# Optimization experiments

Hardware: AMD Instinct MI355X
Metric: run time of the kernel (lower is better)

## Reference

```python
import jax, jax.numpy as jnp
import numpy as np

ALPHA = 0.1
K = 10


def setup_inputs() -> dict:
    key = jax.random.key(0)
    ks = jax.random.split(key, 8)
    N, E, F_IN, H, C = 100000, 1600000, 256, 128, 16
    features = jax.random.normal(ks[0], (N, F_IN), dtype=jnp.float32)
    # Kaiming-ish small init so activations stay sane
    W0 = jax.random.normal(ks[1], (F_IN, H), dtype=jnp.float32) * (1.0 / np.sqrt(F_IN))
    b0 = jnp.zeros((H,), jnp.float32)
    W1 = jax.random.normal(ks[2], (H, H), dtype=jnp.float32) * (1.0 / np.sqrt(H))
    b1 = jnp.zeros((H,), jnp.float32)
    W2 = jax.random.normal(ks[3], (H, C), dtype=jnp.float32) * (1.0 / np.sqrt(H))
    b2 = jnp.zeros((C,), jnp.float32)
    src = jax.random.randint(ks[4], (E,), 0, N, dtype=jnp.int32)
    dst = jax.random.randint(ks[5], (E,), 0, N, dtype=jnp.int32)
    return {"features": features, "W0": W0, "b0": b0, "W1": W1, "b1": b1,
            "W2": W2, "b2": b2, "src": src, "dst": dst}


def reference(features, W0, b0, W1, b1, W2, b2, src, dst):
    N = features.shape[0]
    # --- MLP feature transform (feat_drop=0 -> identity) ---
    h = jax.nn.relu(features @ W0 + b0)
    h = jax.nn.relu(h @ W1 + b1)
    h = h @ W2 + b2  # [N, C]
    # --- symmetric normalization D_out^{-1/2} A D_in^{-1/2} (DGL APPNPConv) ---
    ones = jnp.ones(src.shape[0], dtype=h.dtype)
    out_deg = jax.ops.segment_sum(ones, src, num_segments=N)
    in_deg = jax.ops.segment_sum(ones, dst, num_segments=N)
    norm_src = jnp.where(out_deg > 0, jax.lax.rsqrt(jnp.maximum(out_deg, 1.0)), 0.0)[:, None]
    norm_dst = jnp.where(in_deg > 0, jax.lax.rsqrt(jnp.maximum(in_deg, 1.0)), 0.0)[:, None]
    # --- K-step personalized PageRank propagation (edge_drop=0) ---
    h0 = h
    for _ in range(K):
        msg = (h * norm_src)[src]                         # gather [E, C]
        agg = jax.ops.segment_sum(msg, dst, num_segments=N)  # scatter-add [N, C]
        h = (1.0 - ALPHA) * (agg * norm_dst) + ALPHA * h0
    return h
```

## Files before the change

### kernel.cpp

```cpp
#include <hip/hip_runtime.h>

typedef _Float16 half8 __attribute__((ext_vector_type(8)));
typedef _Float16 half4 __attribute__((ext_vector_type(4)));
typedef float f32x4 __attribute__((ext_vector_type(4)));
typedef unsigned short u16;
typedef unsigned char u8;
typedef unsigned int u32;

constexpr int F_IN = 256;
constexpr int H    = 128;
constexpr int C    = 16;
constexpr int KITER = 10;

constexpr int RANGE = 32768;
constexpr int PCH   = 128;


__global__ __launch_bounds__(256) void hist_k(const int* __restrict__ idx,
                                              u8* __restrict__ partial,
                                              int N, int E, int R, int chunk) {
    __shared__ unsigned int cnt[RANGE / 4];
    const int p  = blockIdx.x / R;
    const int r  = blockIdx.x % R;
    const int lo = r * RANGE;
    const int hi = min(lo + RANGE, N);
    const int t  = threadIdx.x;
    for (int i = t; i < RANGE / 4; i += 256) cnt[i] = 0;
    __syncthreads();
    const int e0 = p * chunk, e1 = min(e0 + chunk, E);
    for (int e = e0 + t; e < e1; e += 256) {
        int d = idx[e];
        if (d >= lo && d < hi) {
            int dl = d - lo;
            atomicAdd(&cnt[dl >> 2], 1u << ((dl & 3) << 3));
        }
    }
    __syncthreads();
    const int nw = (hi - lo) >> 2;
    u8* prow = partial + (size_t)p * N + lo;
    for (int k = t; k < nw; k += 256)
        *reinterpret_cast<u32*>(prow + k * 4) = cnt[k];
    for (int i = lo + nw * 4 + t; i < hi; i += 256) {
        int il = i - lo;
        partial[(size_t)p * N + i] = (u8)(cnt[il >> 2] >> ((il & 3) << 3));
    }
}

__global__ __launch_bounds__(256) void hist_rank_k(const int* __restrict__ idx,
                                                   u8* __restrict__ partial,
                                                   u8* __restrict__ rank8,
                                                   int N, int E, int R, int chunk) {
    __shared__ unsigned int cnt[RANGE / 4];
    const int p  = blockIdx.x / R;
    const int r  = blockIdx.x % R;
    const int lo = r * RANGE;
    const int hi = min(lo + RANGE, N);
    const int t  = threadIdx.x;
    for (int i = t; i < RANGE / 4; i += 256) cnt[i] = 0;
    __syncthreads();
    const int e0 = p * chunk, e1 = min(e0 + chunk, E);
    for (int e = e0 + t; e < e1; e += 256) {
        int d = idx[e];
        if (d >= lo && d < hi) {
            int dl    = d - lo;
            int shift = (dl & 3) << 3;
            unsigned int old = atomicAdd(&cnt[dl >> 2], 1u << shift);
            rank8[e] = (u8)((old >> shift) & 0xffu);
        }
    }
    __syncthreads();
    const int nw = (hi - lo) >> 2;
    u8* prow = partial + (size_t)p * N + lo;
    for (int k = t; k < nw; k += 256)
        *reinterpret_cast<u32*>(prow + k * 4) = cnt[k];
    for (int i = lo + nw * 4 + t; i < hi; i += 256) {
        int il = i - lo;
        partial[(size_t)p * N + i] = (u8)(cnt[il >> 2] >> ((il & 3) << 3));
    }
}


__global__ __launch_bounds__(256) void colsum4_k(const u8* __restrict__ partial,
                                                 int* __restrict__ deg, int NG, int N) {
    int q = blockIdx.x * 256 + threadIdx.x;
    if (q >= NG) return;
    int i0 = q * 4;
    if (i0 + 4 <= N) {
        int s0 = 0, s1 = 0, s2 = 0, s3 = 0;
#pragma unroll 8
        for (int p = 0; p < PCH; ++p) {
            uchar4 v = *reinterpret_cast<const uchar4*>(partial + (size_t)p * N + i0);
            s0 += v.x; s1 += v.y; s2 += v.z; s3 += v.w;
        }
        *reinterpret_cast<int4*>(deg + i0) = make_int4(s0, s1, s2, s3);
    } else {
        for (int i = i0; i < N; ++i) {
            int s = 0;
            for (int p = 0; p < PCH; ++p) s += partial[(size_t)p * N + i];
            deg[i] = s;
        }
    }
}


__global__ __launch_bounds__(256) void colprefix_norm_scan4_k(u8* __restrict__ partial,
                                                              const int* __restrict__ dego,
                                                              float* __restrict__ ns,
                                                              float* __restrict__ nd,
                                                              int* __restrict__ off,
                                                              int* __restrict__ bsum,
                                                              int NG, int N) {
    __shared__ int s[256];
    int t = threadIdx.x, q = blockIdx.x * 256 + t;
    int r0 = 0, r1 = 0, r2 = 0, r3 = 0;
    int i0 = q * 4;
    bool full = (q < NG) && (i0 + 4 <= N);
    if (full) {
        for (int p = 0; p < PCH; ++p) {
            size_t base = (size_t)p * N + i0;
            uchar4 v = *reinterpret_cast<const uchar4*>(partial + base);
            uchar4 w; w.x = (u8)r0; w.y = (u8)r1; w.z = (u8)r2; w.w = (u8)r3;
            *reinterpret_cast<uchar4*>(partial + base) = w;
            r0 += v.x; r1 += v.y; r2 += v.z; r3 += v.w;
        }
        int4 dg = *reinterpret_cast<const int4*>(dego + i0);
        float4 nsv, ndv;
        nsv.x = (dg.x > 0) ? rsqrtf((float)dg.x) : 0.0f;
        nsv.y = (dg.y > 0) ? rsqrtf((float)dg.y) : 0.0f;
        nsv.z = (dg.z > 0) ? rsqrtf((float)dg.z) : 0.0f;
        nsv.w = (dg.w > 0) ? rsqrtf((float)dg.w) : 0.0f;
        ndv.x = (r0 > 0) ? rsqrtf((float)r0) : 0.0f;
        ndv.y = (r1 > 0) ? rsqrtf((float)r1) : 0.0f;
        ndv.z = (r2 > 0) ? rsqrtf((float)r2) : 0.0f;
        ndv.w = (r3 > 0) ? rsqrtf((float)r3) : 0.0f;
        *reinterpret_cast<float4*>(ns + i0) = nsv;
        *reinterpret_cast<float4*>(nd + i0) = ndv;
    } else if (q < NG) {
        int rr[4] = {0, 0, 0, 0};
        int nn = N - i0;
        for (int p = 0; p < PCH; ++p) {
            for (int j = 0; j < nn; ++j) {
                size_t qq = (size_t)p * N + i0 + j;
                int v = partial[qq];
                partial[qq] = (u8)rr[j];
                rr[j] += v;
            }
        }
        for (int j = 0; j < nn; ++j) {
            int a = dego[i0 + j];
            ns[i0 + j] = (a > 0) ? rsqrtf((float)a) : 0.0f;
            nd[i0 + j] = (rr[j] > 0) ? rsqrtf((float)rr[j]) : 0.0f;
        }
        r0 = rr[0]; r1 = rr[1]; r2 = rr[2]; r3 = rr[3];
    }
    int tot = r0 + r1 + r2 + r3;
    s[t] = (q < NG) ? tot : 0;
    __syncthreads();
    for (int dd = 1; dd < 256; dd <<= 1) {
        int x = (t >= dd) ? s[t - dd] : 0;
        __syncthreads();
        s[t] += x;
        __syncthreads();
    }
    if (q < NG) {
        int ex = s[t] - tot;
        if (i0 + 4 <= N) {
            int4 o;
            o.x = ex; o.y = ex + r0; o.z = ex + r0 + r1; o.w = ex + r0 + r1 + r2;
            *reinterpret_cast<int4*>(off + i0) = o;
        } else {
            int rr[4] = {r0, r1, r2, r3};
            int run = ex;
            for (int j = 0; j < N - i0; ++j) { off[i0 + j] = run; run += rr[j]; }
        }
    }
    if (t == 255) bsum[blockIdx.x] = s[255];
}

__global__ __launch_bounds__(512) void scan2(int* __restrict__ bsum, int nb) {
    __shared__ int s[512];
    int t = threadIdx.x;
    int v = (t < nb) ? bsum[t] : 0;
    s[t] = v;
    __syncthreads();
    for (int dd = 1; dd < 512; dd <<= 1) {
        int x = (t >= dd) ? s[t - dd] : 0;
        __syncthreads();
        s[t] += x;
        __syncthreads();
    }
    if (t < nb) bsum[t] = s[t] - v;
}

__global__ __launch_bounds__(256) void scan3_4(int* __restrict__ off, const int* __restrict__ bsum,
                                               int NG, int N) {
    int q = blockIdx.x * 256 + threadIdx.x;
    if (q >= NG) return;
    int b = bsum[blockIdx.x];
    int i0 = q * 4;
    if (i0 + 4 <= N) {
        int4 o = *reinterpret_cast<const int4*>(off + i0);
        o.x += b; o.y += b; o.z += b; o.w += b;
        *reinterpret_cast<int4*>(off + i0) = o;
    } else {
        for (int j = 0; j < N - i0; ++j) off[i0 + j] += b;
    }
}


__global__ __launch_bounds__(256) void scatter_pass(const int* __restrict__ src,
                                                    const int* __restrict__ dst,
                                                    const int* __restrict__ off,
                                                    const u8* __restrict__ pprefix,
                                                    const u8* __restrict__ rank8,
                                                    u32* __restrict__ epack,
                                                    int N, int E, int chunk) {
    int e = blockIdx.x * 256 + threadIdx.x;
    if (e < E) {
        int d = dst[e];
        int p = e / chunk;
        int pos = off[d] + (int)pprefix[(size_t)p * N + d] + (int)rank8[e];
        epack[pos] = (u32)src[e];
    }
}


__device__ inline void pack_one(const float* __restrict__ W, half8* __restrict__ out,
                                int tid, int NT, int Ncols) {
    int l  = tid & 63;
    int q  = tid >> 6;
    int nt = q % NT;
    int ks = q / NT;
    int col = nt * 16 + (l & 15);
    int kb  = ks * 32 + ((l >> 4) * 8);
    half8 h;
#pragma unroll
    for (int j = 0; j < 8; ++j) h[j] = (_Float16)W[(kb + j) * Ncols + col];
    out[tid] = h;
}

__global__ __launch_bounds__(256) void wpack_all(const float* __restrict__ W0,
                                                 const float* __restrict__ W1,
                                                 const float* __restrict__ W2,
                                                 half8* __restrict__ B0,
                                                 half8* __restrict__ B1,
                                                 half8* __restrict__ B2) {
    int tid = blockIdx.x * 256 + threadIdx.x;
    if (tid < 4096)      pack_one(W0, B0, tid, 8, 128);
    else if (tid < 6144) pack_one(W1, B1, tid - 4096, 8, 128);
    else if (tid < 6400) pack_one(W2, B2, tid - 6144, 1, 16);
}


__global__ __launch_bounds__(256) void mlp_direct(
    const float* __restrict__ feat,
    const half8* __restrict__ B0, const float* __restrict__ b0,
    const half8* __restrict__ B1, const float* __restrict__ b1,
    const half8* __restrict__ B2, const float* __restrict__ b2,
    const float* __restrict__ ns,
    float* __restrict__ h0out, _Float16* __restrict__ g0out, int N)
{
    __shared__ __align__(16) char lds[4 * 4096];
    const int t  = threadIdx.x;
    const int l  = t & 63;
    const int w  = t >> 6;
    const int cl = l & 15;
    const int qk = l >> 4;
    char* swp = lds + w * 4096;

    const int rowg = blockIdx.x * 64 + w * 16 + cl;
    const int rowc = (rowg < N) ? rowg : (N - 1);

    const float* ap = feat + (size_t)rowc * F_IN + qk * 8;
    float4 f[16];
#pragma unroll
    for (int i = 0; i < 16; ++i)
        f[i] = *reinterpret_cast<const float4*>(ap + (i >> 1) * 32 + (i & 1) * 4);
    __builtin_amdgcn_sched_barrier(0);

    half8 a0[8];
#pragma unroll
    for (int ks = 0; ks < 8; ++ks) {
        half8 h;
        h[0] = (_Float16)f[2 * ks].x;     h[1] = (_Float16)f[2 * ks].y;
        h[2] = (_Float16)f[2 * ks].z;     h[3] = (_Float16)f[2 * ks].w;
        h[4] = (_Float16)f[2 * ks + 1].x; h[5] = (_Float16)f[2 * ks + 1].y;
        h[6] = (_Float16)f[2 * ks + 1].z; h[7] = (_Float16)f[2 * ks + 1].w;
        a0[ks] = h;
    }

    f32x4 acc0[8];
#pragma unroll
    for (int nt = 0; nt < 8; ++nt) acc0[nt] = (f32x4){0.f, 0.f, 0.f, 0.f};
#pragma unroll
    for (int ks = 0; ks < 8; ++ks)
#pragma unroll
        for (int nt = 0; nt < 8; ++nt)
            acc0[nt] = __builtin_amdgcn_mfma_f32_16x16x32_f16(a0[ks], B0[(ks * 8 + nt) * 64 + l],
                                                              acc0[nt], 0, 0, 0);
#pragma unroll
    for (int nt = 0; nt < 8; ++nt) {
        float bb = b0[nt * 16 + cl];
#pragma unroll
        for (int r = 0; r < 4; ++r) {
            int orow = qk * 4 + r;
            int byte = orow * 256 + (((nt * 16 + cl) * 2) ^ ((orow & 7) << 4));
            *reinterpret_cast<_Float16*>(swp + byte) = (_Float16)fmaxf(acc0[nt][r] + bb, 0.0f);
        }
    }

    half8 a1[4];
#pragma unroll
    for (int ks = 0; ks < 4; ++ks) {
        int byte = cl * 256 + (((qk * 8 + ks * 32) * 2) ^ ((cl & 7) << 4));
        a1[ks] = *reinterpret_cast<const half8*>(swp + byte);
    }
    f32x4 acc1[8];
#pragma unroll
    for (int nt = 0; nt < 8; ++nt) acc1[nt] = (f32x4){0.f, 0.f, 0.f, 0.f};
#pragma unroll
    for (int ks = 0; ks < 4; ++ks)
#pragma unroll
        for (int nt = 0; nt < 8; ++nt)
            acc1[nt] = __builtin_amdgcn_mfma_f32_16x16x32_f16(a1[ks], B1[(ks * 8 + nt) * 64 + l],
                                                              acc1[nt], 0, 0, 0);
#pragma unroll
    for (int nt = 0; nt < 8; ++nt) {
        float bb = b1[nt * 16 + cl];
#pragma unroll
        for (int r = 0; r < 4; ++r) {
            int orow = qk * 4 + r;
            int byte = orow * 256 + (((nt * 16 + cl) * 2) ^ ((orow & 7) << 4));
            *reinterpret_cast<_Float16*>(swp + byte) = (_Float16)fmaxf(acc1[nt][r] + bb, 0.0f);
        }
    }

    f32x4 acc2 = (f32x4){0.f, 0.f, 0.f, 0.f};
#pragma unroll
    for (int ks = 0; ks < 4; ++ks) {
        int byte = cl * 256 + (((qk * 8 + ks * 32) * 2) ^ ((cl & 7) << 4));
        half8 a2 = *reinterpret_cast<const half8*>(swp + byte);
        acc2 = __builtin_amdgcn_mfma_f32_16x16x32_f16(a2, B2[ks * 64 + l], acc2, 0, 0, 0);
    }
    float bb2 = b2[cl];
#pragma unroll
    for (int r = 0; r < 4; ++r) {
        int orow = qk * 4 + r;
        int node = blockIdx.x * 64 + w * 16 + orow;
        if (node < N) {
            float hv = acc2[r] + bb2;
            h0out[(size_t)node * C + cl] = hv;
            g0out[(size_t)node * C + cl] = (_Float16)(hv * ns[node]);
        }
    }
}


__global__ __launch_bounds__(256) void gatherg(const u32* __restrict__ ep,
                                               const int* __restrict__ off,
                                               const half4* __restrict__ g,
                                               const float4* __restrict__ h0,
                                               const float* __restrict__ ns,
                                               const float* __restrict__ nd,
                                               half4* __restrict__ gnext,
                                               float4* __restrict__ hout,
                                               int N, int E, int last) {
    int gid = blockIdx.x * 256 + threadIdx.x;
    int node = gid >> 2;
    if (node >= N) return;
    int c = gid & 3;
    int o0 = off[node];
    int o1 = (node + 1 < N) ? off[node + 1] : E;
    float k  = 0.9f * nd[node];
    float sc = ns[node];
    float4 hv = h0[gid];
    float4 aA = {0.f, 0.f, 0.f, 0.f};
    float4 aB = {0.f, 0.f, 0.f, 0.f};
    float4 aC = {0.f, 0.f, 0.f, 0.f};
    float4 aD = {0.f, 0.f, 0.f, 0.f};
    int o = o0;
    for (; o + 8 <= o1; o += 8) {
        int s0 = (int)ep[o];     int s1 = (int)ep[o + 1];
        int s2 = (int)ep[o + 2]; int s3 = (int)ep[o + 3];
        int s4 = (int)ep[o + 4]; int s5 = (int)ep[o + 5];
        int s6 = (int)ep[o + 6]; int s7 = (int)ep[o + 7];
        half4 x0 = g[s0 * 4 + c]; half4 x1 = g[s1 * 4 + c];
        half4 x2 = g[s2 * 4 + c]; half4 x3 = g[s3 * 4 + c];
        half4 x4 = g[s4 * 4 + c]; half4 x5 = g[s5 * 4 + c];
        half4 x6 = g[s6 * 4 + c]; half4 x7 = g[s7 * 4 + c];
        aA.x += (float)x0[0]; aA.y += (float)x0[1]; aA.z += (float)x0[2]; aA.w += (float)x0[3];
        aB.x += (float)x1[0]; aB.y += (float)x1[1]; aB.z += (float)x1[2]; aB.w += (float)x1[3];
        aC.x += (float)x2[0]; aC.y += (float)x2[1]; aC.z += (float)x2[2]; aC.w += (float)x2[3];
        aD.x += (float)x3[0]; aD.y += (float)x3[1]; aD.z += (float)x3[2]; aD.w += (float)x3[3];
        aA.x += (float)x4[0]; aA.y += (float)x4[1]; aA.z += (float)x4[2]; aA.w += (float)x4[3];
        aB.x += (float)x5[0]; aB.y += (float)x5[1]; aB.z += (float)x5[2]; aB.w += (float)x5[3];
        aC.x += (float)x6[0]; aC.y += (float)x6[1]; aC.z += (float)x6[2]; aC.w += (float)x6[3];
        aD.x += (float)x7[0]; aD.y += (float)x7[1]; aD.z += (float)x7[2]; aD.w += (float)x7[3];
    }
    for (; o + 2 <= o1; o += 2) {
        int s0 = (int)ep[o];
        int s1 = (int)ep[o + 1];
        half4 x0 = g[s0 * 4 + c];
        half4 x1 = g[s1 * 4 + c];
        aA.x += (float)x0[0]; aA.y += (float)x0[1]; aA.z += (float)x0[2]; aA.w += (float)x0[3];
        aB.x += (float)x1[0]; aB.y += (float)x1[1]; aB.z += (float)x1[2]; aB.w += (float)x1[3];
    }
    if (o < o1) {
        int s0 = (int)ep[o];
        half4 x0 = g[s0 * 4 + c];
        aA.x += (float)x0[0]; aA.y += (float)x0[1]; aA.z += (float)x0[2]; aA.w += (float)x0[3];
    }
    aA.x += aB.x + aC.x + aD.x;
    aA.y += aB.y + aC.y + aD.y;
    aA.z += aB.z + aC.z + aD.z;
    aA.w += aB.w + aC.w + aD.w;
    float4 res;
    res.x = fmaf(k, aA.x, 0.1f * hv.x);
    res.y = fmaf(k, aA.y, 0.1f * hv.y);
    res.z = fmaf(k, aA.z, 0.1f * hv.z);
    res.w = fmaf(k, aA.w, 0.1f * hv.w);
    if (last) {
        hout[gid] = res;
    } else {
        half4 gv;
        gv[0] = (_Float16)(res.x * sc);
        gv[1] = (_Float16)(res.y * sc);
        gv[2] = (_Float16)(res.z * sc);
        gv[3] = (_Float16)(res.w * sc);
        gnext[gid] = gv;
    }
}


extern "C" void kernel_launch(void* const* d_in, const int* in_sizes, int n_in,
                              void* d_out, int out_size, void* d_ws, size_t ws_size,
                              hipStream_t stream) {
    const float* feat = (const float*)d_in[0];
    const float* W0   = (const float*)d_in[1];
    const float* b0   = (const float*)d_in[2];
    const float* W1   = (const float*)d_in[3];
    const float* b1   = (const float*)d_in[4];
    const float* W2   = (const float*)d_in[5];
    const float* b2   = (const float*)d_in[6];
    const int*   src  = (const int*)d_in[7];
    const int*   dst  = (const int*)d_in[8];

    const int N = in_sizes[0] / F_IN;
    const int E = in_sizes[7];
    const int R  = (N + RANGE - 1) / RANGE;
    const int chunk = (E + PCH - 1) / PCH;
    const int NG = (N + 3) / 4;
    const int NBG = (NG + 255) / 256;

    char* base = (char*)d_ws;
    u8* part = (u8*)base;
    float*    h0 = (float*)base;
    _Float16* g0 = (_Float16*)(base + (size_t)N * C * 4);
    _Float16* ga = (_Float16*)(base + (size_t)N * C * 6);
    _Float16* gb = (_Float16*)(base + (size_t)N * C * 8);
    char* ws = base + (size_t)N * C * 10;
    int*   dego = (int*)ws;   ws += (size_t)N * 4;
    float* ns   = (float*)ws; ws += (size_t)N * 4;
    float* nd   = (float*)ws; ws += (size_t)N * 4;
    int*   off  = (int*)ws;   ws += (size_t)N * 4;
    int*   bsum = (int*)ws;   ws += 512 * 4;
    u8*    rank8 = (u8*)ws;   ws += (size_t)E;
    ws = (char*)(((size_t)ws + 15) & ~(size_t)15);
    u32*   epack  = (u32*)ws; ws += (size_t)E * 4;
    half8* B0 = (half8*)ws;   ws += 4096 * 16;
    half8* B1 = (half8*)ws;   ws += 2048 * 16;
    half8* B2 = (half8*)ws;   ws += 256 * 16;

    hist_k<<<PCH * R, 256, 0, stream>>>(src, part, N, E, R, chunk);
    colsum4_k<<<NBG, 256, 0, stream>>>(part, dego, NG, N);
    hist_rank_k<<<PCH * R, 256, 0, stream>>>(dst, part, rank8, N, E, R, chunk);
    colprefix_norm_scan4_k<<<NBG, 256, 0, stream>>>(part, dego, ns, nd, off, bsum, NG, N);

    scan2<<<1, 512, 0, stream>>>(bsum, NBG);
    scan3_4<<<NBG, 256, 0, stream>>>(off, bsum, NG, N);
    scatter_pass<<<(E + 255) / 256, 256, 0, stream>>>(src, dst, off, part, rank8, epack, N, E, chunk);

    wpack_all<<<25, 256, 0, stream>>>(W0, W1, W2, B0, B1, B2);
    mlp_direct<<<(N + 63) / 64, 256, 0, stream>>>(feat, B0, b0, B1, b1, B2, b2, ns, h0, g0, N);

    const _Float16* curg = g0;
    for (int it = 0; it < KITER; ++it) {
        int last = (it == KITER - 1);
        _Float16* nxtg = (it & 1) ? gb : ga;
        gatherg<<<(N * 4 + 255) / 256, 256, 0, stream>>>(epack, off, (const half4*)curg,
                                                         (const float4*)h0, ns, nd,
                                                         (half4*)nxtg, (float4*)d_out, N, E, last);
        curg = nxtg;
    }
}
```

Baseline: 323.8 us.

## Sort nodes by in-degree to balance gather work across wavefronts

Adds a counting sort of nodes by in-degree (histogram, scan, scatter kernels) to build a permutation. The propagation gather then processes nodes in degree-sorted order, so lanes in a wavefront run similar loop trip counts and divergence is reduced. The cost is three extra setup kernels, including a serial single-block scan, plus an extra indirection and scattered writes and h0 reads in each iteration.

```diff
diff --git a/kernel.cpp b/kernel.cpp
--- a/kernel.cpp
+++ b/kernel.cpp
@@ -224,6 +224,60 @@
     }
 }
 
+__global__ __launch_bounds__(256) void dhist_k(const int* __restrict__ off,
+                                               u8* __restrict__ rankp,
+                                               int* __restrict__ pbin,
+                                               int NBLK, int N, int E) {
+    __shared__ int hist[256];
+    int t = threadIdx.x, i = blockIdx.x * 256 + t;
+    hist[t] = 0;
+    __syncthreads();
+    if (i < N) {
+        int d = ((i + 1 < N) ? off[i + 1] : E) - off[i];
+        int bin = min(d, 255);
+        int r = atomicAdd(&hist[bin], 1);
+        rankp[i] = (u8)r;
+    }
+    __syncthreads();
+    pbin[(size_t)t * NBLK + blockIdx.x] = hist[t];
+}
+
+__global__ __launch_bounds__(256) void dscan_k(int* __restrict__ pbin,
+                                               int* __restrict__ binb, int NBLK) {
+    __shared__ int s[256];
+    int b = threadIdx.x;
+    int run = 0;
+    for (int k = 0; k < NBLK; ++k) {
+        int v = pbin[(size_t)b * NBLK + k];
+        pbin[(size_t)b * NBLK + k] = run;
+        run += v;
+    }
+    s[b] = run;
+    __syncthreads();
+    for (int dd = 1; dd < 256; dd <<= 1) {
+        int x = (b >= dd) ? s[b - dd] : 0;
+        __syncthreads();
+        s[b] += x;
+        __syncthreads();
+    }
+    binb[b] = s[b] - run;
+}
+
+__global__ __launch_bounds__(256) void dscat_k(const int* __restrict__ off,
+                                               const u8* __restrict__ rankp,
+                                               const int* __restrict__ pbin,
+                                               const int* __restrict__ binb,
+                                               int* __restrict__ perm,
+                                               int NBLK, int N, int E) {
+    int i = blockIdx.x * 256 + threadIdx.x;
+    if (i < N) {
+        int d = ((i + 1 < N) ? off[i + 1] : E) - off[i];
+        int bin = min(d, 255);
+        int pos = binb[bin] + pbin[(size_t)bin * NBLK + blockIdx.x] + (int)rankp[i];
+        perm[pos] = i;
+    }
+}
+
 
 __device__ inline void pack_one(const float* __restrict__ W, half8* __restrict__ out,
                                 int tid, int NT, int Ncols) {
@@ -358,6 +412,7 @@
 
 __global__ __launch_bounds__(256) void gatherg(const u32* __restrict__ ep,
                                                const int* __restrict__ off,
+                                               const int* __restrict__ perm,
                                                const half4* __restrict__ g,
                                                const float4* __restrict__ h0,
                                                const float* __restrict__ ns,
@@ -366,14 +421,16 @@
                                                float4* __restrict__ hout,
                                                int N, int E, int last) {
     int gid = blockIdx.x * 256 + threadIdx.x;
-    int node = gid >> 2;
-    if (node >= N) return;
+    int q = gid >> 2;
+    if (q >= N) return;
+    int node = perm[q];
     int c = gid & 3;
+    int idx4 = node * 4 + c;
     int o0 = off[node];
     int o1 = (node + 1 < N) ? off[node + 1] : E;
     float k  = 0.9f * nd[node];
     float sc = ns[node];
-    float4 hv = h0[gid];
+    float4 hv = h0[idx4];
     float4 aA = {0.f, 0.f, 0.f, 0.f};
     float4 aB = {0.f, 0.f, 0.f, 0.f};
     float4 aC = {0.f, 0.f, 0.f, 0.f};
@@ -420,14 +477,14 @@
     res.z = fmaf(k, aA.z, 0.1f * hv.z);
     res.w = fmaf(k, aA.w, 0.1f * hv.w);
     if (last) {
-        hout[gid] = res;
+        hout[idx4] = res;
     } else {
         half4 gv;
         gv[0] = (_Float16)(res.x * sc);
         gv[1] = (_Float16)(res.y * sc);
         gv[2] = (_Float16)(res.z * sc);
         gv[3] = (_Float16)(res.w * sc);
-        gnext[gid] = gv;
+        gnext[idx4] = gv;
     }
 }
 
@@ -451,6 +508,7 @@
     const int chunk = (E + PCH - 1) / PCH;
     const int NG = (N + 3) / 4;
     const int NBG = (NG + 255) / 256;
+    const int NBLK = (N + 255) / 256;
 
     char* base = (char*)d_ws;
     u8* part = (u8*)base;
@@ -465,8 +523,12 @@
     int*   off  = (int*)ws;   ws += (size_t)N * 4;
     int*   bsum = (int*)ws;   ws += 512 * 4;
     u8*    rank8 = (u8*)ws;   ws += (size_t)E;
+    u8*    rankp = (u8*)ws;   ws += (size_t)N;
     ws = (char*)(((size_t)ws + 15) & ~(size_t)15);
     u32*   epack  = (u32*)ws; ws += (size_t)E * 4;
+    int*   pbin   = (int*)ws; ws += (size_t)256 * NBLK * 4;
+    int*   binb   = (int*)ws; ws += 256 * 4;
+    int*   perm   = (int*)ws; ws += (size_t)N * 4;
     half8* B0 = (half8*)ws;   ws += 4096 * 16;
     half8* B1 = (half8*)ws;   ws += 2048 * 16;
     half8* B2 = (half8*)ws;   ws += 256 * 16;
@@ -480,6 +542,10 @@
     scan3_4<<<NBG, 256, 0, stream>>>(off, bsum, NG, N);
     scatter_pass<<<(E + 255) / 256, 256, 0, stream>>>(src, dst, off, part, rank8, epack, N, E, chunk);
 
+    dhist_k<<<NBLK, 256, 0, stream>>>(off, rankp, pbin, NBLK, N, E);
+    dscan_k<<<1, 256, 0, stream>>>(pbin, binb, NBLK);
+    dscat_k<<<NBLK, 256, 0, stream>>>(off, rankp, pbin, binb, perm, NBLK, N, E);
+
     wpack_all<<<25, 256, 0, stream>>>(W0, W1, W2, B0, B1, B2);
     mlp_direct<<<(N + 63) / 64, 256, 0, stream>>>(feat, B0, b0, B1, b1, B2, b2, ns, h0, g0, N);
 
@@ -487,7 +553,7 @@
     for (int it = 0; it < KITER; ++it) {
         int last = (it == KITER - 1);
         _Float16* nxtg = (it & 1) ? gb : ga;
-        gatherg<<<(N * 4 + 255) / 256, 256, 0, stream>>>(epack, off, (const half4*)curg,
+        gatherg<<<(N * 4 + 255) / 256, 256, 0, stream>>>(epack, off, perm, (const half4*)curg,
                                                          (const float4*)h0, ns, nd,
                                                          (half4*)nxtg, (float4*)d_out, N, E, last);
         curg = nxtg;
```

Measured after the change: 555.5 us. +71.6%, slower.
